# Kernel tuning notes

Hardware: AMD Instinct MI355X
Metric: run time of the kernel (lower is better)

## Reference

```python
import jax, jax.numpy as jnp
import numpy as np

B, S, HID = 1, 2048, 2560
H, HKV, D = 32, 8, 128
G = H // HKV  # GQA group size = 4
EPS = 1e-6
THETA = 1000000.0


def _make_freqs_cis(seq_len, dim, theta):
    inv_freq = 1.0 / (theta ** (np.arange(0, dim, 2, dtype=np.float32) / dim))
    t = np.arange(seq_len, dtype=np.float32)
    ang = np.outer(t, inv_freq)  # [S, D/2]
    emb = np.concatenate([ang, ang], axis=-1)  # [S, D]
    return jnp.asarray(np.stack([np.cos(emb), np.sin(emb)], axis=0))  # [2, S, D]


def setup_inputs() -> dict:
    key = jax.random.key(0)
    ks = jax.random.split(key, 5)
    inp = {
        "hidden_states": jax.random.normal(ks[0], (B, S, HID), dtype=jnp.float32),
        "freqs_cis": _make_freqs_cis(S, D, THETA),
        "Wq": jax.random.normal(ks[1], (H * D, HID), dtype=jnp.float32) * 0.02,
        "Wk": jax.random.normal(ks[2], (HKV * D, HID), dtype=jnp.float32) * 0.02,
        "Wv": jax.random.normal(ks[3], (HKV * D, HID), dtype=jnp.float32) * 0.02,
        "Wo": jax.random.normal(ks[4], (HID, H * D), dtype=jnp.float32) * 0.02,
        "q_norm_w": jnp.ones((D,), dtype=jnp.float32),
        "k_norm_w": jnp.ones((D,), dtype=jnp.float32),
    }
    return inp


def _rms_norm(x, w):
    var = jnp.mean(jnp.square(x), axis=-1, keepdims=True)
    return x * jax.lax.rsqrt(var + EPS) * w


def _rotate_half(x):
    x1, x2 = jnp.split(x, 2, axis=-1)
    return jnp.concatenate([-x2, x1], axis=-1)


def reference(hidden_states, freqs_cis, Wq, Wk, Wv, Wo, q_norm_w, k_norm_w):
    # projections (torch Linear: x @ W.T)
    xq = jnp.einsum('bsh,oh->bso', hidden_states, Wq).reshape(B, S, H, D).swapaxes(1, 2)   # [B,H,S,D]
    xk = jnp.einsum('bsh,oh->bso', hidden_states, Wk).reshape(B, S, HKV, D).swapaxes(1, 2) # [B,Hkv,S,D]
    xv = jnp.einsum('bsh,oh->bso', hidden_states, Wv).reshape(B, S, HKV, D).swapaxes(1, 2)

    # per-head RMSNorm (gemma3-style q/k norm)
    xq = _rms_norm(xq, q_norm_w)
    xk = _rms_norm(xk, k_norm_w)

    # RoPE; cos/sin: [S,D] broadcasts over [B,H,S,D]
    cos, sin = freqs_cis[0], freqs_cis[1]
    xq = xq * cos + _rotate_half(xq) * sin
    xk = xk * cos + _rotate_half(xk) * sin

    # GQA attention without materializing repeated KV: group queries per kv head
    qg = xq.reshape(B, HKV, G, S, D)
    scores = jnp.einsum('bkgqd,bksd->bkgqs', qg, xk) / jnp.sqrt(jnp.asarray(D, xq.dtype))
    probs = jax.nn.softmax(scores, axis=-1)
    out = jnp.einsum('bkgqs,bksd->bkgqd', probs, xv)  # [B,Hkv,G,S,D]

    out = out.reshape(B, H, S, D).swapaxes(1, 2).reshape(B, S, H * D)
    return jnp.einsum('bso,ho->bsh', out, Wo)
```

## Files before the change

kernel.cpp:

```cpp
#include <hip/hip_runtime.h>
#include <stdint.h>

#define S_LEN 2048
#define HID   2560
#define NH    32
#define NKV   8
#define DH    128
#define QD    (NH*DH)
#define KVD   (NKV*DH)

typedef __attribute__((ext_vector_type(8))) short          bf16x8;
typedef __attribute__((ext_vector_type(4))) float          f32x4;
typedef __attribute__((ext_vector_type(8))) unsigned short us8;

static __device__ __forceinline__ unsigned short f2bf(float f) {
  union { float f; uint32_t u; } v; v.f = f;
  uint32_t u = v.u;
  u += 0x7fff + ((u >> 16) & 1);
  return (unsigned short)(u >> 16);
}

static __device__ __forceinline__ void gload16(const void* g, void* l) {
  __builtin_amdgcn_global_load_lds(
      (const __attribute__((address_space(1))) uint32_t*)g,
      (__attribute__((address_space(3))) uint32_t*)l, 16, 0, 0);
}

static __device__ __forceinline__ unsigned cvtpk(float lo, float hi) {
  unsigned r;
  asm volatile("v_cvt_pk_bf16_f32 %0, %1, %2" : "=v"(r) : "v"(lo), "v"(hi));
  return r;
}

__global__ void cast_bf16_k(const float* __restrict__ in,
                            unsigned short* __restrict__ out, int n4) {
  int stride = gridDim.x * blockDim.x;
  for (int i = blockIdx.x * blockDim.x + threadIdx.x; i < n4; i += stride) {
    float4 v = ((const float4*)in)[i];
    ushort4 o;
    o.x = f2bf(v.x); o.y = f2bf(v.y); o.z = f2bf(v.z); o.w = f2bf(v.w);
    ((ushort4*)out)[i] = o;
  }
}

#define BM 128
#define BN 128
#define BK 32

__global__ __launch_bounds__(256)
void gemm_bt(const unsigned short* __restrict__ A,
             const unsigned short* __restrict__ B,
             float* __restrict__ Cf, int M, int N, int K)
{
  __shared__ __align__(16) unsigned short sA[BM * BK];
  __shared__ __align__(16) unsigned short sB[BN * BK];
  const int tid  = threadIdx.x;
  const int wave = tid >> 6, lane = tid & 63;
  const int wr   = wave >> 1, wc = wave & 1;
  const int brow = blockIdx.y, bcol = blockIdx.x;
  const int l15  = lane & 15, lh = lane >> 4;

  f32x4 acc[4][4] = {};

  for (int k0 = 0; k0 < K; k0 += BK) {
    __syncthreads();
#pragma unroll
    for (int c = 0; c < 2; ++c) {
      int chunk = wave * 2 + c;
      int f = chunk * 512 + lane * 8;
      int row = f >> 5, col = f & 31;
      gload16(A + (size_t)(brow * BM + row) * K + k0 + col, (char*)sA + chunk * 1024);
      gload16(B + (size_t)(bcol * BN + row) * K + k0 + col, (char*)sB + chunk * 1024);
    }
    __syncthreads();

    bf16x8 af[4], bfr[4];
#pragma unroll
    for (int i = 0; i < 4; ++i)
      af[i] = *(const bf16x8*)((const char*)sA + (wr * 64 + i * 16 + l15) * 64 + lh * 16);
#pragma unroll
    for (int j = 0; j < 4; ++j)
      bfr[j] = *(const bf16x8*)((const char*)sB + (wc * 64 + j * 16 + l15) * 64 + lh * 16);
#pragma unroll
    for (int i = 0; i < 4; ++i)
#pragma unroll
      for (int j = 0; j < 4; ++j)
        acc[i][j] = __builtin_amdgcn_mfma_f32_16x16x32_bf16(af[i], bfr[j], acc[i][j], 0, 0, 0);
  }

#pragma unroll
  for (int i = 0; i < 4; ++i)
#pragma unroll
    for (int j = 0; j < 4; ++j) {
      int row = brow * BM + wr * 64 + i * 16 + lh * 4;
      int col = bcol * BN + wc * 64 + j * 16 + l15;
#pragma unroll
      for (int r = 0; r < 4; ++r)
        Cf[(size_t)(row + r) * N + col] = acc[i][j][r];
    }
}

__global__ __launch_bounds__(256)
void gemm_qkv(const unsigned short* __restrict__ A,
              const unsigned short* __restrict__ B,
              const float* __restrict__ freqs,
              const float* __restrict__ qw, const float* __restrict__ kw,
              unsigned short* __restrict__ Qo,
              unsigned short* __restrict__ Ko,
              unsigned short* __restrict__ Vo)
{
  __shared__ __align__(16) unsigned short sA[BM * BK];
  __shared__ __align__(16) unsigned short sB[BN * BK];
  const int tid  = threadIdx.x;
  const int wave = tid >> 6, lane = tid & 63;
  const int brow = blockIdx.y, bcol = blockIdx.x;
  const int l15  = lane & 15, lh = lane >> 4;

  f32x4 acc[2][8] = {};

  for (int k0 = 0; k0 < HID; k0 += BK) {
    __syncthreads();
#pragma unroll
    for (int c = 0; c < 2; ++c) {
      int chunk = wave * 2 + c;
      int f = chunk * 512 + lane * 8;
      int row = f >> 5, col = f & 31;
      gload16(A + (size_t)(brow * BM + row) * HID + k0 + col, (char*)sA + chunk * 1024);
      gload16(B + (size_t)(bcol * BN + row) * HID + k0 + col, (char*)sB + chunk * 1024);
    }
    __syncthreads();

    bf16x8 af[2], bfr[8];
#pragma unroll
    for (int i = 0; i < 2; ++i)
      af[i] = *(const bf16x8*)((const char*)sA + (wave * 32 + i * 16 + l15) * 64 + lh * 16);
#pragma unroll
    for (int j = 0; j < 8; ++j)
      bfr[j] = *(const bf16x8*)((const char*)sB + (j * 16 + l15) * 64 + lh * 16);
#pragma unroll
    for (int i = 0; i < 2; ++i)
#pragma unroll
      for (int j = 0; j < 8; ++j)
        acc[i][j] = __builtin_amdgcn_mfma_f32_16x16x32_bf16(af[i], bfr[j], acc[i][j], 0, 0, 0);
  }

  const int ncol0  = bcol * BN;
  const int region = (ncol0 < QD) ? 0 : (ncol0 < QD + KVD ? 1 : 2);
  const float* nw  = (region == 0) ? qw : kw;

#pragma unroll
  for (int i = 0; i < 2; ++i) {
#pragma unroll
    for (int r = 0; r < 4; ++r) {
      int s = brow * BM + wave * 32 + i * 16 + lh * 4 + r;
      float v[8];
#pragma unroll
      for (int j = 0; j < 8; ++j) v[j] = acc[i][j][r];
      if (region < 2) {
        float ss = 0.f;
#pragma unroll
        for (int j = 0; j < 8; ++j) ss += v[j] * v[j];
        ss += __shfl_xor(ss, 1); ss += __shfl_xor(ss, 2);
        ss += __shfl_xor(ss, 4); ss += __shfl_xor(ss, 8);
        float rsq = rsqrtf(ss * (1.0f / 128.0f) + 1e-6f);
        float y[8];
#pragma unroll
        for (int j = 0; j < 8; ++j) y[j] = v[j] * rsq * nw[j * 16 + l15];
        const float* cr = freqs + (size_t)s * DH;
        const float* sr = freqs + (size_t)(S_LEN + s) * DH;
#pragma unroll
        for (int j = 0; j < 4; ++j) {
          int d1 = j * 16 + l15, d2 = (j + 4) * 16 + l15;
          v[j]     = y[j]     * cr[d1] - y[j + 4] * sr[d1];
          v[j + 4] = y[j + 4] * cr[d2] + y[j]     * sr[d2];
        }
      }
      unsigned short* dst;
      if (region == 0)      dst = Qo + (size_t)s * QD  + ncol0;
      else if (region == 1) dst = Ko + (size_t)s * KVD + (ncol0 - QD);
      else                  dst = Vo + (size_t)s * KVD + (ncol0 - QD - KVD);
#pragma unroll
      for (int j = 0; j < 8; ++j) dst[j * 16 + l15] = f2bf(v[j]);
    }
  }
}

__global__ __launch_bounds__(256, 2)
void attn2_k(const unsigned short* __restrict__ Q,
             const unsigned short* __restrict__ Kb,
             const unsigned short* __restrict__ Vb,
             unsigned short* __restrict__ O)
{
  const float SCALE = 0.08838834764831845f;
  const float L2E   = 1.4426950408889634f;
  __shared__ __align__(16) unsigned short sK[2][64 * 128];
  __shared__ __align__(16) unsigned short sV[2][128][72];

  const int kvh  = blockIdx.y;
  const int q0   = blockIdx.x * 32;
  const int wave = threadIdx.x >> 6, lane = threadIdx.x & 63;
  const int l15  = lane & 15, lh = lane >> 4;
  const int h    = kvh * 4 + wave;
  const int vc0  = wave * 32;

  bf16x8 qf[2][4];
#pragma unroll
  for (int qt = 0; qt < 2; ++qt) {
    const unsigned short* qp = Q + (size_t)(q0 + qt * 16 + l15) * QD + h * DH + lh * 8;
#pragma unroll
    for (int kk = 0; kk < 4; ++kk) qf[qt][kk] = *(const bf16x8*)(qp + kk * 32);
  }

  f32x4 oacc[2][8] = {};
  float m_q[2] = { -1e30f, -1e30f }, l_q[2] = { 0.f, 0.f };

  auto stageK = [&](int b, int t0) {
#pragma unroll
    for (int c = 0; c < 4; ++c) {
      int chunk = wave * 4 + c;
      int fb = chunk * 1024 + lane * 16;
      int row = fb >> 8;
      int gi = (fb & 255) ^ ((row & 7) << 4);
      gload16(Kb + (size_t)(t0 + row) * KVD + kvh * DH + (gi >> 1),
              (char*)sK[b] + chunk * 1024);
    }
  };
  auto loadV = [&](us8* vv, int t0) {
    const unsigned short* vsrc = Vb + (size_t)(t0 + lane) * KVD + kvh * DH + vc0;
#pragma unroll
    for (int u = 0; u < 4; ++u) vv[u] = *(const us8*)(vsrc + u * 8);
  };
  auto writeV = [&](int b, const us8* vv) {
#pragma unroll
    for (int u = 0; u < 4; ++u)
#pragma unroll
      for (int k = 0; k < 8; ++k)
        sV[b][vc0 + u * 8 + k][lane] = (unsigned short)vv[u][k];
  };

  {
    us8 vv[4];
    stageK(0, 0);
    loadV(vv, 0);
    writeV(0, vv);
  }
  asm volatile("s_waitcnt vmcnt(0)" ::: "memory");
  __syncthreads();
  int buf = 0;

  const int srcA = (lh & 1) * 32 + l15;
  const int srcB = srcA + 16;
  const bool thi = (lh >> 1) != 0;

  for (int t = 0; t < S_LEN / 64; ++t) {
    const bool pre = (t + 1 < S_LEN / 64);
    us8 vv[4];
    if (pre) { stageK(buf ^ 1, (t + 1) * 64); loadV(vv, (t + 1) * 64); }

    f32x4 sacc[2][4] = {};
#pragma unroll
    for (int kk = 0; kk < 4; ++kk) {
      bf16x8 kf[4];
#pragma unroll
      for (int tt = 0; tt < 4; ++tt) {
        int krow = tt * 16 + l15;
        kf[tt] = *(const bf16x8*)((const char*)sK[buf] + krow * 256 +
                                  ((kk * 64 + lh * 16) ^ ((krow & 7) << 4)));
      }
#pragma unroll
      for (int tt = 0; tt < 4; ++tt) {
        sacc[0][tt] = __builtin_amdgcn_mfma_f32_16x16x32_bf16(kf[tt], qf[0][kk], sacc[0][tt], 0, 0, 0);
        sacc[1][tt] = __builtin_amdgcn_mfma_f32_16x16x32_bf16(kf[tt], qf[1][kk], sacc[1][tt], 0, 0, 0);
      }
    }

    unsigned pk[2][4][2];
    float corr[2];
#pragma unroll
    for (int qt = 0; qt < 2; ++qt) {
      float mx = sacc[qt][0][0];
#pragma unroll
      for (int tt = 0; tt < 4; ++tt)
#pragma unroll
        for (int r = 0; r < 4; ++r) mx = fmaxf(mx, sacc[qt][tt][r]);
      mx = fmaxf(mx, __shfl_xor(mx, 16));
      mx = fmaxf(mx, __shfl_xor(mx, 32));
      float mn = fmaxf(m_q[qt], mx * SCALE);
      corr[qt] = exp2f((m_q[qt] - mn) * L2E);
      m_q[qt] = mn;
      float sum = 0.f;
      float p[4][4];
#pragma unroll
      for (int tt = 0; tt < 4; ++tt)
#pragma unroll
        for (int r = 0; r < 4; ++r) {
          p[tt][r] = exp2f((sacc[qt][tt][r] * SCALE - mn) * L2E);
          sum += p[tt][r];
        }
      sum += __shfl_xor(sum, 16);
      sum += __shfl_xor(sum, 32);
      l_q[qt] = l_q[qt] * corr[qt] + sum;
#pragma unroll
      for (int tt = 0; tt < 4; ++tt) {
        pk[qt][tt][0] = cvtpk(p[tt][0], p[tt][1]);
        pk[qt][tt][1] = cvtpk(p[tt][2], p[tt][3]);
      }
    }

    bf16x8 pfrag[2][2];
#pragma unroll
    for (int qt = 0; qt < 2; ++qt)
#pragma unroll
      for (int kk2 = 0; kk2 < 2; ++kk2) {
        union { unsigned w[4]; bf16x8 v; } u;
        int ta = 2 * kk2, tb = 2 * kk2 + 1;
        unsigned a, b;
        a = (unsigned)__shfl((int)pk[qt][ta][0], srcA); b = (unsigned)__shfl((int)pk[qt][tb][0], srcA);
        u.w[0] = thi ? b : a;
        a = (unsigned)__shfl((int)pk[qt][ta][1], srcA); b = (unsigned)__shfl((int)pk[qt][tb][1], srcA);
        u.w[1] = thi ? b : a;
        a = (unsigned)__shfl((int)pk[qt][ta][0], srcB); b = (unsigned)__shfl((int)pk[qt][tb][0], srcB);
        u.w[2] = thi ? b : a;
        a = (unsigned)__shfl((int)pk[qt][ta][1], srcB); b = (unsigned)__shfl((int)pk[qt][tb][1], srcB);
        u.w[3] = thi ? b : a;
        pfrag[qt][kk2] = u.v;
      }

    if (pre) writeV(buf ^ 1, vv);

#pragma unroll
    for (int qt = 0; qt < 2; ++qt)
#pragma unroll
      for (int dt = 0; dt < 8; ++dt)
#pragma unroll
        for (int r = 0; r < 4; ++r) oacc[qt][dt][r] *= corr[qt];

#pragma unroll
    for (int dt = 0; dt < 8; ++dt) {
#pragma unroll
      for (int kk2 = 0; kk2 < 2; ++kk2) {
        bf16x8 vf = *(const bf16x8*)&sV[buf][dt * 16 + l15][kk2 * 32 + lh * 8];
        oacc[0][dt] = __builtin_amdgcn_mfma_f32_16x16x32_bf16(vf, pfrag[0][kk2], oacc[0][dt], 0, 0, 0);
        oacc[1][dt] = __builtin_amdgcn_mfma_f32_16x16x32_bf16(vf, pfrag[1][kk2], oacc[1][dt], 0, 0, 0);
      }
    }

    asm volatile("s_waitcnt vmcnt(0)" ::: "memory");
    __syncthreads();
    buf ^= 1;
  }

#pragma unroll
  for (int qt = 0; qt < 2; ++qt) {
    float inv = 1.0f / l_q[qt];
    size_t row = (size_t)(q0 + qt * 16 + l15) * QD + h * DH;
#pragma unroll
    for (int dt = 0; dt < 8; ++dt) {
      ushort4 o;
      o.x = f2bf(oacc[qt][dt][0] * inv);
      o.y = f2bf(oacc[qt][dt][1] * inv);
      o.z = f2bf(oacc[qt][dt][2] * inv);
      o.w = f2bf(oacc[qt][dt][3] * inv);
      *(ushort4*)(O + row + dt * 16 + lh * 4) = o;
    }
  }
}

extern "C" void kernel_launch(void* const* d_in, const int* in_sizes, int n_in,
                              void* d_out, int out_size, void* d_ws, size_t ws_size,
                              hipStream_t stream)
{
  const float* hs    = (const float*)d_in[0];
  const float* freqs = (const float*)d_in[1];
  const float* Wq    = (const float*)d_in[2];
  const float* Wk    = (const float*)d_in[3];
  const float* Wv    = (const float*)d_in[4];
  const float* Wo    = (const float*)d_in[5];
  const float* qw    = (const float*)d_in[6];
  const float* kw    = (const float*)d_in[7];
  float* out = (float*)d_out;

  char* ws = (char*)d_ws;
  size_t off = 0;
  auto alloc = [&](size_t bytes) {
    char* p = ws + off;
    off += (bytes + 255) & ~(size_t)255;
    return p;
  };
  unsigned short* hs_b   = (unsigned short*)alloc((size_t)S_LEN * HID * 2);
  unsigned short* wqkv_b = (unsigned short*)alloc((size_t)(QD + 2 * KVD) * HID * 2);
  unsigned short* Wo_b   = (unsigned short*)alloc((size_t)HID * QD * 2);
  unsigned short* q_b    = (unsigned short*)alloc((size_t)S_LEN * QD * 2);
  unsigned short* k_b    = (unsigned short*)alloc((size_t)S_LEN * KVD * 2);
  unsigned short* v_b    = (unsigned short*)alloc((size_t)S_LEN * KVD * 2);
  unsigned short* at_b   = (unsigned short*)alloc((size_t)S_LEN * QD * 2);

  auto cast = [&](const float* src, unsigned short* dst, int n) {
    int n4 = n / 4;
    int blocks = (n4 + 255) / 256; if (blocks > 2048) blocks = 2048;
    cast_bf16_k<<<dim3(blocks), dim3(256), 0, stream>>>(src, dst, n4);
  };
  cast(hs, hs_b, S_LEN * HID);
  cast(Wq, wqkv_b,                       QD * HID);
  cast(Wk, wqkv_b + (size_t)QD * HID,    KVD * HID);
  cast(Wv, wqkv_b + (size_t)(QD + KVD) * HID, KVD * HID);
  cast(Wo, Wo_b, HID * QD);

  gemm_qkv<<<dim3((QD + 2 * KVD) / BN, S_LEN / BM), dim3(256), 0, stream>>>(
      hs_b, wqkv_b, freqs, qw, kw, q_b, k_b, v_b);

  attn2_k<<<dim3(S_LEN / 32, NKV), dim3(256), 0, stream>>>(q_b, k_b, v_b, at_b);

  gemm_bt<<<dim3(HID / BN, S_LEN / BM), dim3(256), 0, stream>>>(
      at_b, Wo_b, out, S_LEN, HID, QD);
}
```

Baseline: 521.9 us.

## Switch attention MFMAs to 32x32x16 tiles with permlane32 swap for P fragments

Rewrites the flash-attention inner loop to use 32x32x16 bf16 MFMAs instead of 16x16x32. Each lane now owns one query row, which cuts the cross-lane max/sum reductions to one shuffle. The P-to-A-operand relayout uses v_permlane32_swap instead of many __shfl calls, and the scale and log2e factors are folded into one multiply. It also adds s_setprio around the MFMA sections. The aim is fewer LDS reads per FLOP and less shuffle and VALU overhead, at the risk of higher register pressure from 16-wide accumulators.

```diff
diff --git a/kernel.cpp b/kernel.cpp
--- a/kernel.cpp
+++ b/kernel.cpp
@@ -9,9 +9,10 @@
 #define QD    (NH*DH)
 #define KVD   (NKV*DH)
 
-typedef __attribute__((ext_vector_type(8))) short          bf16x8;
-typedef __attribute__((ext_vector_type(4))) float          f32x4;
-typedef __attribute__((ext_vector_type(8))) unsigned short us8;
+typedef __attribute__((ext_vector_type(8)))  short          bf16x8;
+typedef __attribute__((ext_vector_type(4)))  float          f32x4;
+typedef __attribute__((ext_vector_type(16))) float          f32x16;
+typedef __attribute__((ext_vector_type(8)))  unsigned short us8;
 
 static __device__ __forceinline__ unsigned short f2bf(float f) {
   union { float f; uint32_t u; } v; v.f = f;
@@ -30,6 +31,10 @@
   unsigned r;
   asm volatile("v_cvt_pk_bf16_f32 %0, %1, %2" : "=v"(r) : "v"(lo), "v"(hi));
   return r;
+}
+
+static __device__ __forceinline__ void plswap(unsigned& a, unsigned& b) {
+  asm volatile("v_permlane32_swap_b32 %0, %1" : "+v"(a), "+v"(b));
 }
 
 __global__ void cast_bf16_k(const float* __restrict__ in,
@@ -191,28 +196,26 @@
              const unsigned short* __restrict__ Vb,
              unsigned short* __restrict__ O)
 {
-  const float SCALE = 0.08838834764831845f;
-  const float L2E   = 1.4426950408889634f;
+  const float SC = 0.08838834764831845f * 1.4426950408889634f;
   __shared__ __align__(16) unsigned short sK[2][64 * 128];
   __shared__ __align__(16) unsigned short sV[2][128][72];
 
   const int kvh  = blockIdx.y;
   const int q0   = blockIdx.x * 32;
   const int wave = threadIdx.x >> 6, lane = threadIdx.x & 63;
-  const int l15  = lane & 15, lh = lane >> 4;
+  const int l31  = lane & 31, half = lane >> 5;
   const int h    = kvh * 4 + wave;
   const int vc0  = wave * 32;
 
-  bf16x8 qf[2][4];
-#pragma unroll
-  for (int qt = 0; qt < 2; ++qt) {
-    const unsigned short* qp = Q + (size_t)(q0 + qt * 16 + l15) * QD + h * DH + lh * 8;
-#pragma unroll
-    for (int kk = 0; kk < 4; ++kk) qf[qt][kk] = *(const bf16x8*)(qp + kk * 32);
-  }
-
-  f32x4 oacc[2][8] = {};
-  float m_q[2] = { -1e30f, -1e30f }, l_q[2] = { 0.f, 0.f };
+  bf16x8 qf[8];
+  {
+    const unsigned short* qp = Q + (size_t)(q0 + l31) * QD + h * DH + half * 8;
+#pragma unroll
+    for (int ds = 0; ds < 8; ++ds) qf[ds] = *(const bf16x8*)(qp + ds * 16);
+  }
+
+  f32x16 oacc[4] = {};
+  float m_c = -1e30f, l_c = 0.f;
 
   auto stageK = [&](int b, int t0) {
 #pragma unroll
@@ -248,121 +251,98 @@
   __syncthreads();
   int buf = 0;
 
-  const int srcA = (lh & 1) * 32 + l15;
-  const int srcB = srcA + 16;
-  const bool thi = (lh >> 1) != 0;
-
   for (int t = 0; t < S_LEN / 64; ++t) {
     const bool pre = (t + 1 < S_LEN / 64);
     us8 vv[4];
     if (pre) { stageK(buf ^ 1, (t + 1) * 64); loadV(vv, (t + 1) * 64); }
 
-    f32x4 sacc[2][4] = {};
-#pragma unroll
-    for (int kk = 0; kk < 4; ++kk) {
-      bf16x8 kf[4];
-#pragma unroll
-      for (int tt = 0; tt < 4; ++tt) {
-        int krow = tt * 16 + l15;
-        kf[tt] = *(const bf16x8*)((const char*)sK[buf] + krow * 256 +
-                                  ((kk * 64 + lh * 16) ^ ((krow & 7) << 4)));
-      }
-#pragma unroll
-      for (int tt = 0; tt < 4; ++tt) {
-        sacc[0][tt] = __builtin_amdgcn_mfma_f32_16x16x32_bf16(kf[tt], qf[0][kk], sacc[0][tt], 0, 0, 0);
-        sacc[1][tt] = __builtin_amdgcn_mfma_f32_16x16x32_bf16(kf[tt], qf[1][kk], sacc[1][tt], 0, 0, 0);
-      }
-    }
-
-    unsigned pk[2][4][2];
-    float corr[2];
-#pragma unroll
-    for (int qt = 0; qt < 2; ++qt) {
-      float mx = sacc[qt][0][0];
-#pragma unroll
-      for (int tt = 0; tt < 4; ++tt)
-#pragma unroll
-        for (int r = 0; r < 4; ++r) mx = fmaxf(mx, sacc[qt][tt][r]);
-      mx = fmaxf(mx, __shfl_xor(mx, 16));
-      mx = fmaxf(mx, __shfl_xor(mx, 32));
-      float mn = fmaxf(m_q[qt], mx * SCALE);
-      corr[qt] = exp2f((m_q[qt] - mn) * L2E);
-      m_q[qt] = mn;
-      float sum = 0.f;
-      float p[4][4];
-#pragma unroll
-      for (int tt = 0; tt < 4; ++tt)
-#pragma unroll
-        for (int r = 0; r < 4; ++r) {
-          p[tt][r] = exp2f((sacc[qt][tt][r] * SCALE - mn) * L2E);
-          sum += p[tt][r];
-        }
-      sum += __shfl_xor(sum, 16);
-      sum += __shfl_xor(sum, 32);
-      l_q[qt] = l_q[qt] * corr[qt] + sum;
-#pragma unroll
-      for (int tt = 0; tt < 4; ++tt) {
-        pk[qt][tt][0] = cvtpk(p[tt][0], p[tt][1]);
-        pk[qt][tt][1] = cvtpk(p[tt][2], p[tt][3]);
-      }
-    }
-
-    bf16x8 pfrag[2][2];
-#pragma unroll
-    for (int qt = 0; qt < 2; ++qt)
-#pragma unroll
-      for (int kk2 = 0; kk2 < 2; ++kk2) {
+    f32x16 sm[2] = {};
+    __builtin_amdgcn_s_setprio(1);
+#pragma unroll
+    for (int kc = 0; kc < 2; ++kc) {
+      int krow = kc * 32 + l31;
+      int rb = krow * 256, sw = (krow & 7) << 4;
+#pragma unroll
+      for (int ds = 0; ds < 8; ++ds) {
+        bf16x8 kf = *(const bf16x8*)((const char*)sK[buf] + rb + ((ds * 32 + half * 16) ^ sw));
+        sm[kc] = __builtin_amdgcn_mfma_f32_32x32x16_bf16(kf, qf[ds], sm[kc], 0, 0, 0);
+      }
+    }
+    __builtin_amdgcn_s_setprio(0);
+
+    float mraw = sm[0][0];
+#pragma unroll
+    for (int kc = 0; kc < 2; ++kc)
+#pragma unroll
+      for (int r = 0; r < 16; ++r) mraw = fmaxf(mraw, sm[kc][r]);
+    mraw = fmaxf(mraw, __shfl_xor(mraw, 32));
+    float mn = fmaxf(m_c, mraw * SC);
+    float corr = exp2f(m_c - mn);
+    m_c = mn;
+
+    float p[2][16];
+    float sum = 0.f;
+#pragma unroll
+    for (int kc = 0; kc < 2; ++kc)
+#pragma unroll
+      for (int r = 0; r < 16; ++r) {
+        p[kc][r] = exp2f(sm[kc][r] * SC - mn);
+        sum += p[kc][r];
+      }
+    sum += __shfl_xor(sum, 32);
+    l_c = l_c * corr + sum;
+
+    bf16x8 pfrag[4];
+#pragma unroll
+    for (int kc = 0; kc < 2; ++kc)
+#pragma unroll
+      for (int ksl = 0; ksl < 2; ++ksl) {
+        int rb = ksl * 8;
+        unsigned x0 = cvtpk(p[kc][rb + 0], p[kc][rb + 1]);
+        unsigned y0 = cvtpk(p[kc][rb + 4], p[kc][rb + 5]);
+        unsigned x1 = cvtpk(p[kc][rb + 2], p[kc][rb + 3]);
+        unsigned y1 = cvtpk(p[kc][rb + 6], p[kc][rb + 7]);
+        plswap(x0, y0);
+        plswap(x1, y1);
         union { unsigned w[4]; bf16x8 v; } u;
-        int ta = 2 * kk2, tb = 2 * kk2 + 1;
-        unsigned a, b;
-        a = (unsigned)__shfl((int)pk[qt][ta][0], srcA); b = (unsigned)__shfl((int)pk[qt][tb][0], srcA);
-        u.w[0] = thi ? b : a;
-        a = (unsigned)__shfl((int)pk[qt][ta][1], srcA); b = (unsigned)__shfl((int)pk[qt][tb][1], srcA);
-        u.w[1] = thi ? b : a;
-        a = (unsigned)__shfl((int)pk[qt][ta][0], srcB); b = (unsigned)__shfl((int)pk[qt][tb][0], srcB);
-        u.w[2] = thi ? b : a;
-        a = (unsigned)__shfl((int)pk[qt][ta][1], srcB); b = (unsigned)__shfl((int)pk[qt][tb][1], srcB);
-        u.w[3] = thi ? b : a;
-        pfrag[qt][kk2] = u.v;
+        u.w[0] = x0; u.w[1] = x1; u.w[2] = y0; u.w[3] = y1;
+        pfrag[kc * 2 + ksl] = u.v;
       }
 
     if (pre) writeV(buf ^ 1, vv);
 
 #pragma unroll
-    for (int qt = 0; qt < 2; ++qt)
-#pragma unroll
-      for (int dt = 0; dt < 8; ++dt)
-#pragma unroll
-        for (int r = 0; r < 4; ++r) oacc[qt][dt][r] *= corr[qt];
-
-#pragma unroll
-    for (int dt = 0; dt < 8; ++dt) {
-#pragma unroll
-      for (int kk2 = 0; kk2 < 2; ++kk2) {
-        bf16x8 vf = *(const bf16x8*)&sV[buf][dt * 16 + l15][kk2 * 32 + lh * 8];
-        oacc[0][dt] = __builtin_amdgcn_mfma_f32_16x16x32_bf16(vf, pfrag[0][kk2], oacc[0][dt], 0, 0, 0);
-        oacc[1][dt] = __builtin_amdgcn_mfma_f32_16x16x32_bf16(vf, pfrag[1][kk2], oacc[1][dt], 0, 0, 0);
-      }
-    }
+    for (int dt = 0; dt < 4; ++dt)
+#pragma unroll
+      for (int r = 0; r < 16; ++r) oacc[dt][r] *= corr;
+
+    __builtin_amdgcn_s_setprio(1);
+#pragma unroll
+    for (int dt = 0; dt < 4; ++dt) {
+#pragma unroll
+      for (int ks = 0; ks < 4; ++ks) {
+        bf16x8 vfa = *(const bf16x8*)&sV[buf][dt * 32 + l31][ks * 16 + half * 8];
+        oacc[dt] = __builtin_amdgcn_mfma_f32_32x32x16_bf16(vfa, pfrag[ks], oacc[dt], 0, 0, 0);
+      }
+    }
+    __builtin_amdgcn_s_setprio(0);
 
     asm volatile("s_waitcnt vmcnt(0)" ::: "memory");
     __syncthreads();
     buf ^= 1;
   }
 
-#pragma unroll
-  for (int qt = 0; qt < 2; ++qt) {
-    float inv = 1.0f / l_q[qt];
-    size_t row = (size_t)(q0 + qt * 16 + l15) * QD + h * DH;
-#pragma unroll
-    for (int dt = 0; dt < 8; ++dt) {
-      ushort4 o;
-      o.x = f2bf(oacc[qt][dt][0] * inv);
-      o.y = f2bf(oacc[qt][dt][1] * inv);
-      o.z = f2bf(oacc[qt][dt][2] * inv);
-      o.w = f2bf(oacc[qt][dt][3] * inv);
-      *(ushort4*)(O + row + dt * 16 + lh * 4) = o;
-    }
+  {
+    float inv = 1.0f / l_c;
+    unsigned short* orow = O + (size_t)(q0 + l31) * QD + h * DH;
+#pragma unroll
+    for (int dt = 0; dt < 4; ++dt)
+#pragma unroll
+      for (int r = 0; r < 16; r += 2) {
+        int d = dt * 32 + (r & 3) + 8 * (r >> 2) + 4 * half;
+        unsigned w = cvtpk(oacc[dt][r] * inv, oacc[dt][r + 1] * inv);
+        *(unsigned*)(orow + d) = w;
+      }
   }
 }
 
```

After: 501.6 us. 1.04x faster.
